# Kernel tuning notes

Hardware: AMD Instinct MI355X
Metric: run time of the kernel (lower is better)

## Reference

```python
import jax, jax.numpy as jnp
import numpy as np

N_NODES = 100000
N_EDGES = 3200000
D_FEAT = 64


def setup_inputs() -> dict:
    key = jax.random.key(0)
    k1, k2, k3 = jax.random.split(key, 3)
    x = jax.random.normal(k1, (N_NODES, D_FEAT), dtype=jnp.float32)
    up_index = jax.random.randint(k2, (2, N_EDGES), 0, N_NODES, dtype=jnp.int64)
    down_index = jax.random.randint(k3, (2, N_EDGES), 0, N_NODES, dtype=jnp.int64)
    return {"x": x, "up_index": up_index, "down_index": down_index}


def _propagate(x, edge_index, num_nodes):
    # flow = 'source_to_target': (i, j) = (1, 0)
    # __lift__: gather x along node_dim=-2 at source indices (row j=0)
    msg = x[edge_index[0]]                      # [E, D]  message_up(x_j) = x_j
    # aggregate 'add': scatter-add messages to target indices (row i=1)
    return jax.ops.segment_sum(msg, edge_index[1], num_segments=num_nodes)  # [N, D]


def reference(x, up_index, down_index):
    up_out = _propagate(x, up_index, x.shape[0])
    down_out = _propagate(x, down_index, x.shape[0])
    # update: combine up and down aggregations (identity update -> sum)
    return up_out + down_out
```

## Files before the change

kernel.cpp:

```cpp
#include <hip/hip_runtime.h>


static constexpr int D = 64;
static constexpr int Q = 16;
static constexpr int NPB = 64;
static constexpr int NPB_SHIFT = 6;
static constexpr int CHUNK = 4096;
static constexpr int CH = 4096;
static constexpr int MAXT = 32;

__global__ void detect_idx_dtype(const int* __restrict__ w, int* __restrict__ flag) {
    int tid = threadIdx.x;
    int v = w[2 * tid + 1];
    unsigned long long m = __ballot(v != 0);
    if (tid == 0) *flag = (m == 0ULL) ? 1 : 0;
}

__device__ __forceinline__ int load_idx_nt(const void* idx, long long i, int is64) {
    return is64 ? (int)__builtin_nontemporal_load(((const long long*)idx) + i)
                : __builtin_nontemporal_load(((const int*)idx) + i);
}

__global__ __launch_bounds__(256) void bucket_hist_kernel(
        const void* __restrict__ up, const void* __restrict__ down,
        int* __restrict__ bcounts, const int* __restrict__ flag, int E, int NB) {
    extern __shared__ int lcnt[];
    const int is64 = *flag;
    for (int i = threadIdx.x; i < NB; i += blockDim.x) lcnt[i] = 0;
    __syncthreads();
    const long long total = 2LL * E;
    const long long stride = (long long)gridDim.x * blockDim.x;
    for (long long e = (long long)blockIdx.x * blockDim.x + threadIdx.x;
         e < total; e += stride) {
        const void* idx = up; long long ee = e;
        if (ee >= E) { idx = down; ee -= E; }
        int dst = load_idx_nt(idx, E + ee, is64);
        atomicAdd(&lcnt[dst >> NPB_SHIFT], 1);
    }
    __syncthreads();
    for (int i = threadIdx.x; i < NB; i += blockDim.x)
        if (lcnt[i]) atomicAdd(&bcounts[i], lcnt[i]);
}

__global__ __launch_bounds__(1024) void scan_kernel(
        const int* __restrict__ counts, int* __restrict__ offsets,
        int* __restrict__ cursors, int NB) {
    __shared__ int sums[1024];
    const int tid = threadIdx.x;
    const int chunk = (NB + 1023) / 1024;
    const int start = tid * chunk;
    const int end = min(start + chunk, NB);
    int s = 0;
    for (int i = start; i < end; i++) s += counts[i];
    sums[tid] = s;
    __syncthreads();
    for (int off = 1; off < 1024; off <<= 1) {
        int t = (tid >= off) ? sums[tid - off] : 0;
        __syncthreads();
        sums[tid] += t;
        __syncthreads();
    }
    int run = (tid == 0) ? 0 : sums[tid - 1];
    for (int i = start; i < end; i++) {
        offsets[i] = run;
        cursors[i] = run;
        run += counts[i];
    }
    if (tid == 1023) offsets[NB] = run;
}

__global__ __launch_bounds__(256) void bucket_scatter_kernel(
        const void* __restrict__ up, const void* __restrict__ down,
        int* __restrict__ gcursor, unsigned* __restrict__ packed,
        const int* __restrict__ flag, int E, int NB) {
    extern __shared__ int lds[];
    int* cnt = lds;
    int* base = lds + NB;
    const int is64 = *flag;
    const long long total = 2LL * E;
    const long long cs = (long long)blockIdx.x * CHUNK;
    if (cs >= total) return;
    const int m = (int)(min(total, cs + (long long)CHUNK) - cs);
    const int tid = threadIdx.x;

    for (int i = tid; i < NB; i += 256) cnt[i] = 0;
    __syncthreads();

    unsigned pr[16];
    int bkt[16];
    #pragma unroll
    for (int k = 0; k < 16; k++) {
        const int i = tid + (k << 8);
        bkt[k] = -1;
        if (i < m) {
            long long e = cs + i;
            const void* idx = up; long long ee = e;
            if (ee >= E) { idx = down; ee -= E; }
            const int src = load_idx_nt(idx, ee, is64);
            const int dst = load_idx_nt(idx, E + ee, is64);
            pr[k] = ((unsigned)src << NPB_SHIFT) | (unsigned)(dst & (NPB - 1));
            bkt[k] = dst >> NPB_SHIFT;
            atomicAdd(&cnt[bkt[k]], 1);
        }
    }
    __syncthreads();
    for (int i = tid; i < NB; i += 256) {
        int c = cnt[i];
        base[i] = c ? atomicAdd(&gcursor[i], c) : 0;
        cnt[i] = 0;
    }
    __syncthreads();
    #pragma unroll
    for (int k = 0; k < 16; k++) {
        if (bkt[k] >= 0) {
            int pos = base[bkt[k]] + atomicAdd(&cnt[bkt[k]], 1);
            packed[pos] = pr[k];
        }
    }
}

__global__ __launch_bounds__(256) void bucket_gather_kernel(
        const float* __restrict__ x, const int* __restrict__ offsets,
        const unsigned* __restrict__ packed, float* __restrict__ out,
        int N, int shift, int NT) {
    extern __shared__ int lds[];
    unsigned* sorted = (unsigned*)lds;
    int* cnt = lds + CH;
    int* binoff = cnt + NT * NPB;
    const int nbins = NT * NPB;

    const int b = blockIdx.x;
    const int tid = threadIdx.x;
    const int g = tid >> 4;
    const int q = tid & 15;
    const int beg = offsets[b], end = offsets[b + 1];
    const float* xq = x + q * 4;

    float4 acc0 = make_float4(0.f, 0.f, 0.f, 0.f);
    float4 acc1 = acc0, acc2 = acc0, acc3 = acc0;

    for (int cs = beg; cs < end; cs += CH) {
        const int m = min(CH, end - cs);
        for (int i = tid; i < nbins; i += 256) cnt[i] = 0;
        __syncthreads();
        unsigned pr[16];
        #pragma unroll
        for (int k = 0; k < 16; k++) {
            const int i = tid + (k << 8);
            if (i < m) {
                unsigned p = __builtin_nontemporal_load(packed + cs + i);
                pr[k] = p;
                int key = (int)(p & (NPB - 1)) * NT + (int)(p >> (NPB_SHIFT + shift));
                atomicAdd(&cnt[key], 1);
            }
        }
        __syncthreads();
        if (tid < 64) {
            const int K = (nbins + 63) >> 6;
            const int base = tid * K;
            int S = 0;
            for (int k = 0; k < K; k++) {
                int i = base + k;
                if (i < nbins) S += cnt[i];
            }
            int inc = S;
            #pragma unroll
            for (int off = 1; off < 64; off <<= 1) {
                int t = __shfl_up(inc, off, 64);
                if (tid >= off) inc += t;
            }
            int run = inc - S;
            for (int k = 0; k < K; k++) {
                int i = base + k;
                if (i < nbins) {
                    int c = cnt[i];
                    cnt[i] = run;
                    binoff[i + 1] = run + c;
                    run += c;
                }
            }
            if (tid == 0) binoff[0] = 0;
        }
        __syncthreads();
        #pragma unroll
        for (int k = 0; k < 16; k++) {
            const int i = tid + (k << 8);
            if (i < m) {
                unsigned p = pr[k];
                int key = (int)(p & (NPB - 1)) * NT + (int)(p >> (NPB_SHIFT + shift));
                int pos = atomicAdd(&cnt[key], 1);
                sorted[pos] = p;
            }
        }
        __syncthreads();

#define GATHER_NODE(ACC, J) do {                                               \
        const int dl = 4 * g + (J);                                            \
        const int rb = binoff[dl * NT], re = binoff[(dl + 1) * NT];            \
        int e = rb;                                                            \
        for (; e + 8 <= re; e += 8) {                                          \
            const unsigned p0 = sorted[e + 0], p1 = sorted[e + 1];             \
            const unsigned p2 = sorted[e + 2], p3 = sorted[e + 3];             \
            const unsigned p4 = sorted[e + 4], p5 = sorted[e + 5];             \
            const unsigned p6 = sorted[e + 6], p7 = sorted[e + 7];             \
            const float4 v0 = *(const float4*)(xq + ((long long)(p0 >> NPB_SHIFT)) * D); \
            const float4 v1 = *(const float4*)(xq + ((long long)(p1 >> NPB_SHIFT)) * D); \
            const float4 v2 = *(const float4*)(xq + ((long long)(p2 >> NPB_SHIFT)) * D); \
            const float4 v3 = *(const float4*)(xq + ((long long)(p3 >> NPB_SHIFT)) * D); \
            const float4 v4 = *(const float4*)(xq + ((long long)(p4 >> NPB_SHIFT)) * D); \
            const float4 v5 = *(const float4*)(xq + ((long long)(p5 >> NPB_SHIFT)) * D); \
            const float4 v6 = *(const float4*)(xq + ((long long)(p6 >> NPB_SHIFT)) * D); \
            const float4 v7 = *(const float4*)(xq + ((long long)(p7 >> NPB_SHIFT)) * D); \
            ACC.x += ((v0.x + v1.x) + (v2.x + v3.x)) + ((v4.x + v5.x) + (v6.x + v7.x)); \
            ACC.y += ((v0.y + v1.y) + (v2.y + v3.y)) + ((v4.y + v5.y) + (v6.y + v7.y)); \
            ACC.z += ((v0.z + v1.z) + (v2.z + v3.z)) + ((v4.z + v5.z) + (v6.z + v7.z)); \
            ACC.w += ((v0.w + v1.w) + (v2.w + v3.w)) + ((v4.w + v5.w) + (v6.w + v7.w)); \
        }                                                                      \
        for (; e < re; e++) {                                                  \
            const unsigned p = sorted[e];                                      \
            const float4 v = *(const float4*)(xq + ((long long)(p >> NPB_SHIFT)) * D); \
            ACC.x += v.x; ACC.y += v.y; ACC.z += v.z; ACC.w += v.w;            \
        }                                                                      \
    } while (0)

        GATHER_NODE(acc0, 0);
        GATHER_NODE(acc1, 1);
        GATHER_NODE(acc2, 2);
        GATHER_NODE(acc3, 3);
#undef GATHER_NODE
        __syncthreads();
    }

    const int node0 = b * NPB + 4 * g;
    if (node0 < N)
        *(float4*)(out + (long long)node0 * D + q * 4) = acc0;
    if (node0 + 1 < N)
        *(float4*)(out + (long long)(node0 + 1) * D + q * 4) = acc1;
    if (node0 + 2 < N)
        *(float4*)(out + (long long)(node0 + 2) * D + q * 4) = acc2;
    if (node0 + 3 < N)
        *(float4*)(out + (long long)(node0 + 3) * D + q * 4) = acc3;
}

__global__ __launch_bounds__(256) void scatter_add_kernel(
        const float* __restrict__ x, const void* __restrict__ up_idx,
        const void* __restrict__ down_idx, float* __restrict__ out,
        const int* __restrict__ dtype_flag, int num_edges) {
    const int is64 = *dtype_flag;
    const long long total = 2LL * num_edges * Q;
    const long long stride = (long long)gridDim.x * blockDim.x;
    for (long long t = (long long)blockIdx.x * blockDim.x + threadIdx.x;
         t < total; t += stride) {
        const int quad = (int)(t & (Q - 1));
        long long eg = t >> 4;
        const void* idx = up_idx;
        if (eg >= num_edges) { idx = down_idx; eg -= num_edges; }
        int src = load_idx_nt(idx, eg, is64);
        int dst = load_idx_nt(idx, num_edges + eg, is64);
        const float4 v = *(const float4*)(x + (long long)src * D + quad * 4);
        float* o = out + (long long)dst * D + quad * 4;
        unsafeAtomicAdd(o + 0, v.x);
        unsafeAtomicAdd(o + 1, v.y);
        unsafeAtomicAdd(o + 2, v.z);
        unsafeAtomicAdd(o + 3, v.w);
    }
}

extern "C" void kernel_launch(void* const* d_in, const int* in_sizes, int n_in,
                              void* d_out, int out_size, void* d_ws, size_t ws_size,
                              hipStream_t stream) {
    const float* x = (const float*)d_in[0];
    const void* up_idx = d_in[1];
    const void* down_idx = d_in[2];
    float* out = (float*)d_out;

    const int E = in_sizes[1] / 2;
    const int N = out_size / D;
    const int NB = (N + NPB - 1) / NPB;
    const long long Etot = 2LL * E;

    int shift = 13;
    while ((((long long)(N - 1) >> shift) + 1) > MAXT) shift++;
    const int NT = (int)(((long long)(N - 1) >> shift) + 1);

    int* ws_i = (int*)d_ws;
    int* flag = ws_i;
    int* counts = ws_i + 64;
    int* offsets = counts + NB;
    int* cursors = offsets + NB + 15;
    unsigned* packed = (unsigned*)(cursors + NB);
    const size_t ws_need = (size_t)(64 + 3LL * NB + 16 + Etot) * 4 + 64;

    detect_idx_dtype<<<1, 64, 0, stream>>>((const int*)up_idx, flag);

    if (ws_size >= ws_need && N <= (1 << 25) && Etot < (1LL << 31)) {
        hipMemsetAsync(counts, 0, (size_t)NB * sizeof(int), stream);
        bucket_hist_kernel<<<1024, 256, NB * sizeof(int), stream>>>(
            up_idx, down_idx, counts, flag, E, NB);
        scan_kernel<<<1, 1024, 0, stream>>>(counts, offsets, cursors, NB);
        const int sblocks = (int)((Etot + CHUNK - 1) / CHUNK);
        bucket_scatter_kernel<<<sblocks, 256, 2 * NB * sizeof(int), stream>>>(
            up_idx, down_idx, cursors, packed, flag, E, NB);
        const int nbins = NT * NPB;
        const size_t glds = (size_t)(CH + 2 * nbins + 4) * 4;
        bucket_gather_kernel<<<NB, 256, glds, stream>>>(
            x, offsets, packed, out, N, shift, NT);
    } else {
        hipMemsetAsync(d_out, 0, (size_t)out_size * sizeof(float), stream);
        scatter_add_kernel<<<8192, 256, 0, stream>>>(x, up_idx, down_idx, out, flag, E);
    }
}
```

Baseline: 481.5 us.

## Reorder gather bins source-tile-major and interleave four node streams

The in-block sort key now places the source tile in the high bits and the local destination node in the low bits. The gather loop then walks each source tile and processes four destination nodes together, two edges each, so more independent loads are in flight and concurrent accesses land in the same x region. The scatter kernel moves to 512 threads with an 8192-edge chunk, and the histogram kernel gets twice as many blocks. The interleaved loop needs extra drain loops for uneven bin lengths and loops over NT tiles, which adds some control overhead.

```diff
diff --git a/kernel.cpp b/kernel.cpp
--- a/kernel.cpp
+++ b/kernel.cpp
@@ -5,7 +5,7 @@
 static constexpr int Q = 16;
 static constexpr int NPB = 64;
 static constexpr int NPB_SHIFT = 6;
-static constexpr int CHUNK = 4096;
+static constexpr int CHUNK = 8192;
 static constexpr int CH = 4096;
 static constexpr int MAXT = 32;
 
@@ -69,7 +69,7 @@
     if (tid == 1023) offsets[NB] = run;
 }
 
-__global__ __launch_bounds__(256) void bucket_scatter_kernel(
+__global__ __launch_bounds__(512) void bucket_scatter_kernel(
         const void* __restrict__ up, const void* __restrict__ down,
         int* __restrict__ gcursor, unsigned* __restrict__ packed,
         const int* __restrict__ flag, int E, int NB) {
@@ -83,14 +83,14 @@
     const int m = (int)(min(total, cs + (long long)CHUNK) - cs);
     const int tid = threadIdx.x;
 
-    for (int i = tid; i < NB; i += 256) cnt[i] = 0;
+    for (int i = tid; i < NB; i += 512) cnt[i] = 0;
     __syncthreads();
 
     unsigned pr[16];
     int bkt[16];
     #pragma unroll
     for (int k = 0; k < 16; k++) {
-        const int i = tid + (k << 8);
+        const int i = tid + (k << 9);
         bkt[k] = -1;
         if (i < m) {
             long long e = cs + i;
@@ -104,7 +104,7 @@
         }
     }
     __syncthreads();
-    for (int i = tid; i < NB; i += 256) {
+    for (int i = tid; i < NB; i += 512) {
         int c = cnt[i];
         base[i] = c ? atomicAdd(&gcursor[i], c) : 0;
         cnt[i] = 0;
@@ -139,6 +139,22 @@
     float4 acc0 = make_float4(0.f, 0.f, 0.f, 0.f);
     float4 acc1 = acc0, acc2 = acc0, acc3 = acc0;
 
+#define LOAD1(E) (*(const float4*)(xq + ((long long)(sorted[E] >> NPB_SHIFT)) * D))
+#define DRAIN(A, E, RE) do {                                                   \
+        for (; (E) + 4 <= (RE); (E) += 4) {                                    \
+            const float4 w0 = LOAD1((E) + 0), w1 = LOAD1((E) + 1);             \
+            const float4 w2 = LOAD1((E) + 2), w3 = LOAD1((E) + 3);             \
+            A.x += (w0.x + w1.x) + (w2.x + w3.x);                              \
+            A.y += (w0.y + w1.y) + (w2.y + w3.y);                              \
+            A.z += (w0.z + w1.z) + (w2.z + w3.z);                              \
+            A.w += (w0.w + w1.w) + (w2.w + w3.w);                              \
+        }                                                                      \
+        for (; (E) < (RE); (E)++) {                                            \
+            const float4 w = LOAD1(E);                                         \
+            A.x += w.x; A.y += w.y; A.z += w.z; A.w += w.w;                    \
+        }                                                                      \
+    } while (0)
+
     for (int cs = beg; cs < end; cs += CH) {
         const int m = min(CH, end - cs);
         for (int i = tid; i < nbins; i += 256) cnt[i] = 0;
@@ -150,7 +166,7 @@
             if (i < m) {
                 unsigned p = __builtin_nontemporal_load(packed + cs + i);
                 pr[k] = p;
-                int key = (int)(p & (NPB - 1)) * NT + (int)(p >> (NPB_SHIFT + shift));
+                int key = (int)((p >> (NPB_SHIFT + shift)) << NPB_SHIFT) | (int)(p & (NPB - 1));
                 atomicAdd(&cnt[key], 1);
             }
         }
@@ -187,49 +203,42 @@
             const int i = tid + (k << 8);
             if (i < m) {
                 unsigned p = pr[k];
-                int key = (int)(p & (NPB - 1)) * NT + (int)(p >> (NPB_SHIFT + shift));
+                int key = (int)((p >> (NPB_SHIFT + shift)) << NPB_SHIFT) | (int)(p & (NPB - 1));
                 int pos = atomicAdd(&cnt[key], 1);
                 sorted[pos] = p;
             }
         }
         __syncthreads();
 
-#define GATHER_NODE(ACC, J) do {                                               \
-        const int dl = 4 * g + (J);                                            \
-        const int rb = binoff[dl * NT], re = binoff[(dl + 1) * NT];            \
-        int e = rb;                                                            \
-        for (; e + 8 <= re; e += 8) {                                          \
-            const unsigned p0 = sorted[e + 0], p1 = sorted[e + 1];             \
-            const unsigned p2 = sorted[e + 2], p3 = sorted[e + 3];             \
-            const unsigned p4 = sorted[e + 4], p5 = sorted[e + 5];             \
-            const unsigned p6 = sorted[e + 6], p7 = sorted[e + 7];             \
-            const float4 v0 = *(const float4*)(xq + ((long long)(p0 >> NPB_SHIFT)) * D); \
-            const float4 v1 = *(const float4*)(xq + ((long long)(p1 >> NPB_SHIFT)) * D); \
-            const float4 v2 = *(const float4*)(xq + ((long long)(p2 >> NPB_SHIFT)) * D); \
-            const float4 v3 = *(const float4*)(xq + ((long long)(p3 >> NPB_SHIFT)) * D); \
-            const float4 v4 = *(const float4*)(xq + ((long long)(p4 >> NPB_SHIFT)) * D); \
-            const float4 v5 = *(const float4*)(xq + ((long long)(p5 >> NPB_SHIFT)) * D); \
-            const float4 v6 = *(const float4*)(xq + ((long long)(p6 >> NPB_SHIFT)) * D); \
-            const float4 v7 = *(const float4*)(xq + ((long long)(p7 >> NPB_SHIFT)) * D); \
-            ACC.x += ((v0.x + v1.x) + (v2.x + v3.x)) + ((v4.x + v5.x) + (v6.x + v7.x)); \
-            ACC.y += ((v0.y + v1.y) + (v2.y + v3.y)) + ((v4.y + v5.y) + (v6.y + v7.y)); \
-            ACC.z += ((v0.z + v1.z) + (v2.z + v3.z)) + ((v4.z + v5.z) + (v6.z + v7.z)); \
-            ACC.w += ((v0.w + v1.w) + (v2.w + v3.w)) + ((v4.w + v5.w) + (v6.w + v7.w)); \
-        }                                                                      \
-        for (; e < re; e++) {                                                  \
-            const unsigned p = sorted[e];                                      \
-            const float4 v = *(const float4*)(xq + ((long long)(p >> NPB_SHIFT)) * D); \
-            ACC.x += v.x; ACC.y += v.y; ACC.z += v.z; ACC.w += v.w;            \
-        }                                                                      \
-    } while (0)
-
-        GATHER_NODE(acc0, 0);
-        GATHER_NODE(acc1, 1);
-        GATHER_NODE(acc2, 2);
-        GATHER_NODE(acc3, 3);
-#undef GATHER_NODE
-        __syncthreads();
-    }
+        for (int t = 0; t < NT; t++) {
+            const int kb = t * NPB + 4 * g;
+            const int c0 = binoff[kb], c1 = binoff[kb + 1], c2 = binoff[kb + 2];
+            const int c3 = binoff[kb + 3], c4 = binoff[kb + 4];
+            int e0 = c0, e1 = c1, e2 = c2, e3 = c3;
+            while (e0 + 2 <= c1 && e1 + 2 <= c2 && e2 + 2 <= c3 && e3 + 2 <= c4) {
+                const float4 u0 = LOAD1(e0), u1 = LOAD1(e0 + 1);
+                const float4 u2 = LOAD1(e1), u3 = LOAD1(e1 + 1);
+                const float4 u4 = LOAD1(e2), u5 = LOAD1(e2 + 1);
+                const float4 u6 = LOAD1(e3), u7 = LOAD1(e3 + 1);
+                acc0.x += u0.x + u1.x; acc0.y += u0.y + u1.y;
+                acc0.z += u0.z + u1.z; acc0.w += u0.w + u1.w;
+                acc1.x += u2.x + u3.x; acc1.y += u2.y + u3.y;
+                acc1.z += u2.z + u3.z; acc1.w += u2.w + u3.w;
+                acc2.x += u4.x + u5.x; acc2.y += u4.y + u5.y;
+                acc2.z += u4.z + u5.z; acc2.w += u4.w + u5.w;
+                acc3.x += u6.x + u7.x; acc3.y += u6.y + u7.y;
+                acc3.z += u6.z + u7.z; acc3.w += u6.w + u7.w;
+                e0 += 2; e1 += 2; e2 += 2; e3 += 2;
+            }
+            DRAIN(acc0, e0, c1);
+            DRAIN(acc1, e1, c2);
+            DRAIN(acc2, e2, c3);
+            DRAIN(acc3, e3, c4);
+        }
+        __syncthreads();
+    }
+#undef DRAIN
+#undef LOAD1
 
     const int node0 = b * NPB + 4 * g;
     if (node0 < N)
@@ -295,11 +304,11 @@
 
     if (ws_size >= ws_need && N <= (1 << 25) && Etot < (1LL << 31)) {
         hipMemsetAsync(counts, 0, (size_t)NB * sizeof(int), stream);
-        bucket_hist_kernel<<<1024, 256, NB * sizeof(int), stream>>>(
+        bucket_hist_kernel<<<2048, 256, NB * sizeof(int), stream>>>(
             up_idx, down_idx, counts, flag, E, NB);
         scan_kernel<<<1, 1024, 0, stream>>>(counts, offsets, cursors, NB);
         const int sblocks = (int)((Etot + CHUNK - 1) / CHUNK);
-        bucket_scatter_kernel<<<sblocks, 256, 2 * NB * sizeof(int), stream>>>(
+        bucket_scatter_kernel<<<sblocks, 512, 2 * NB * sizeof(int), stream>>>(
             up_idx, down_idx, cursors, packed, flag, E, NB);
         const int nbins = NT * NPB;
         const size_t glds = (size_t)(CH + 2 * nbins + 4) * 4;
```

Result: no change. 482.2 us (+0.1%).
